# Kernel optimization log

Hardware: AMD Instinct MI355X
Metric: run time of the kernel (lower is better)

## Reference

```python
import jax, jax.numpy as jnp
import numpy as np

B, H, S, D = 4, 16, 2048, 64

def setup_inputs() -> dict:
    key = jax.random.key(0)
    kq, kk, kv = jax.random.split(key, 3)
    q = jax.random.normal(kq, (B, H, S, D), dtype=jnp.float32)
    k = jax.random.normal(kk, (B, H, S, D), dtype=jnp.float32)
    v = jax.random.normal(kv, (B, H, S, D), dtype=jnp.float32)
    return {"q": q, "k": k, "v": v}

def reference(q, k, v):
    # naive unfused attention: scores = QK^T / sqrt(d), softmax, then @ V
    scale = 1.0 / jnp.sqrt(jnp.asarray(q.shape[-1], q.dtype))
    scores = jnp.einsum('bhqd,bhkd->bhqk', q, k) * scale  # [B,H,S,S] materialized
    attn = jax.nn.softmax(scores, axis=-1)
    out = jnp.einsum('bhqk,bhkd->bhqd', attn, v)
    return out
```

## Files before the change

kernel.cpp:

```cpp
#include <hip/hip_runtime.h>


#define S_LEN 2048
#define D_DIM 64
#define N_BH  64
#define QSCALE 0.18033688011112042f

typedef _Float16 half8 __attribute__((ext_vector_type(8)));
typedef _Float16 half4 __attribute__((ext_vector_type(4)));
typedef float floatx16 __attribute__((ext_vector_type(16)));
typedef unsigned int uint4v __attribute__((ext_vector_type(4)));

#define MFMA32(a, b, c) __builtin_amdgcn_mfma_f32_32x32x16_f16((a), (b), (c), 0, 0, 0)

#define GLL16(g, l) __builtin_amdgcn_global_load_lds(                      \
    (const __attribute__((address_space(1))) void*)(g),                    \
    (__attribute__((address_space(3))) void*)(l), 16, 0, 0)

__global__ __launch_bounds__(256) void prep_kernel(
    const float* __restrict__ kg, const float* __restrict__ vg,
    _Float16* __restrict__ kh, _Float16* __restrict__ vt)
{
    __shared__ _Float16 Ls[64 * 132];
    const int tid = threadIdx.x;
    const int bh = blockIdx.y;
    const int sbase = blockIdx.x * 128;
    const size_t gbase = ((size_t)(bh * S_LEN + sbase)) * D_DIM;

#pragma unroll
    for (int i = 0; i < 8; ++i) {
        const int e = i * 1024 + tid * 4;
        const float4 kv = *(const float4*)(kg + gbase + e);
        half4 hk;
        hk[0] = (_Float16)kv.x; hk[1] = (_Float16)kv.y;
        hk[2] = (_Float16)kv.z; hk[3] = (_Float16)kv.w;
        *(half4*)(kh + gbase + e) = hk;
    }
#pragma unroll
    for (int i = 0; i < 8; ++i) {
        const int e = i * 1024 + tid * 4;
        const int s = e >> 6, d0 = e & 63;
        const float4 vv = *(const float4*)(vg + gbase + e);
        const int sp = (s & ~12) | ((s & 4) << 1) | ((s & 8) >> 1);
        Ls[(d0 + 0) * 132 + sp] = (_Float16)vv.x;
        Ls[(d0 + 1) * 132 + sp] = (_Float16)vv.y;
        Ls[(d0 + 2) * 132 + sp] = (_Float16)vv.z;
        Ls[(d0 + 3) * 132 + sp] = (_Float16)vv.w;
    }
    __syncthreads();
    const int w = tid >> 6, L = tid & 63;
    const int dr = L >> 4;
    const int c  = L & 15;
#pragma unroll
    for (int k = 0; k < 4; ++k) {
        const int d = w * 16 + k * 4 + dr;
        const half4 lo = *(const half4*)&Ls[d * 132 + c * 8];
        const half4 hi = *(const half4*)&Ls[d * 132 + c * 8 + 4];
        half8 o;
        o[0] = lo[0]; o[1] = lo[1]; o[2] = lo[2]; o[3] = lo[3];
        o[4] = hi[0]; o[5] = hi[1]; o[6] = hi[2]; o[7] = hi[3];
        *(half8*)(vt + ((size_t)(bh * D_DIM + d)) * S_LEN + sbase + c * 8) = o;
    }
}

__global__ __launch_bounds__(256, 2) void fa_kernel(
    const float* __restrict__ qg, const _Float16* __restrict__ kh,
    const _Float16* __restrict__ vt, float* __restrict__ outg)
{
    __shared__ _Float16 Kl0[64 * 64];
    __shared__ _Float16 Kl1[64 * 64];
    __shared__ _Float16 Vl0[64 * 64];
    __shared__ _Float16 Vl1[64 * 64];

    const int tid = threadIdx.x;
    const int w = tid >> 6;
    const int L = tid & 63;
    const int lq = L & 31;
    const int h = L >> 5;

    const int id = blockIdx.x;
    const int bh   = ((id & 7) << 3) | (id >> 6);
    const int qblk = (id >> 3) & 7;
    const int qrowA = qblk * 256 + w * 32 + lq;

    half8 qbA[4], qbB[4];
    {
        const float* qpA = qg + ((size_t)bh * S_LEN + qrowA) * D_DIM + h * 8;
        const float* qpB = qpA + 128 * D_DIM;
#pragma unroll
        for (int ks = 0; ks < 4; ++ks) {
            const float4 a0 = *(const float4*)(qpA + ks * 16);
            const float4 b0 = *(const float4*)(qpA + ks * 16 + 4);
            const float4 a1 = *(const float4*)(qpB + ks * 16);
            const float4 b1 = *(const float4*)(qpB + ks * 16 + 4);
            qbA[ks][0] = (_Float16)(a0.x * QSCALE);
            qbA[ks][1] = (_Float16)(a0.y * QSCALE);
            qbA[ks][2] = (_Float16)(a0.z * QSCALE);
            qbA[ks][3] = (_Float16)(a0.w * QSCALE);
            qbA[ks][4] = (_Float16)(b0.x * QSCALE);
            qbA[ks][5] = (_Float16)(b0.y * QSCALE);
            qbA[ks][6] = (_Float16)(b0.z * QSCALE);
            qbA[ks][7] = (_Float16)(b0.w * QSCALE);
            qbB[ks][0] = (_Float16)(a1.x * QSCALE);
            qbB[ks][1] = (_Float16)(a1.y * QSCALE);
            qbB[ks][2] = (_Float16)(a1.z * QSCALE);
            qbB[ks][3] = (_Float16)(a1.w * QSCALE);
            qbB[ks][4] = (_Float16)(b1.x * QSCALE);
            qbB[ks][5] = (_Float16)(b1.y * QSCALE);
            qbB[ks][6] = (_Float16)(b1.z * QSCALE);
            qbB[ks][7] = (_Float16)(b1.w * QSCALE);
        }
    }

    floatx16 o0A, o1A, lacA, o0B, o1B, lacB;
#pragma unroll
    for (int r = 0; r < 16; ++r) {
        o0A[r] = 0.f; o1A[r] = 0.f; lacA[r] = 0.f;
        o0B[r] = 0.f; o1B[r] = 0.f; lacB[r] = 0.f;
    }

    half8 ones;
#pragma unroll
    for (int j = 0; j < 8; ++j) ones[j] = (_Float16)1.0f;

    const int rloc = L >> 3, lc = L & 7;
    const int crd = lc ^ rloc;
    const _Float16* kgl = kh + (size_t)bh * S_LEN * D_DIM
                        + (size_t)(w * 16 + rloc) * D_DIM + crd * 8;
    const _Float16* vgl = vt + (size_t)bh * D_DIM * S_LEN
                        + (size_t)(w * 16 + rloc) * S_LEN + crd * 8;
    const int woff = w * 16 * 64;

#define STAGE(KD, VD) do {                                                 \
        GLL16(kgl,                     &KD[woff]);                         \
        GLL16(kgl + (size_t)8 * D_DIM, &KD[woff + 8 * 64]);                \
        GLL16(vgl,                     &VD[woff]);                         \
        GLL16(vgl + (size_t)8 * S_LEN, &VD[woff + 8 * 64]);                \
        kgl += 64 * D_DIM;                                                 \
        vgl += 64;                                                         \
    } while (0)

#define COMPUTE(KB, VB) do {                                               \
                 \
        floatx16 s0A, s1A, s0B, s1B;                                       \
        _Pragma("unroll")                                                  \
        for (int r = 0; r < 16; ++r) {                                     \
            s0A[r] = 0.f; s1A[r] = 0.f; s0B[r] = 0.f; s1B[r] = 0.f;        \
        }                                                                  \
        __builtin_amdgcn_s_setprio(1);                                     \
        _Pragma("unroll")                                                  \
        for (int ks = 0; ks < 4; ++ks) {                                   \
            const int sw = (((2 * ks + h) ^ (lq & 7)) << 3);               \
            const half8 ka0 = *(const half8*)&KB[lq * 64 + sw];            \
            const half8 ka1 = *(const half8*)&KB[(32 + lq) * 64 + sw];     \
            s0A = MFMA32(ka0, qbA[ks], s0A);                               \
            s1A = MFMA32(ka1, qbA[ks], s1A);                               \
            s0B = MFMA32(ka0, qbB[ks], s0B);                               \
            s1B = MFMA32(ka1, qbB[ks], s1B);                               \
        }                                                                  \
        __builtin_amdgcn_s_setprio(0);                                     \
                           \
        unsigned int pkA0[8], pkA1[8], pkB0[8], pkB1[8];                   \
        _Pragma("unroll")                                                  \
        for (int p = 0; p < 8; ++p) {                                      \
            const auto eA0 = __builtin_amdgcn_cvt_pkrtz(                   \
                __builtin_amdgcn_exp2f(s0A[2 * p]),                        \
                __builtin_amdgcn_exp2f(s0A[2 * p + 1]));                   \
            const auto eA1 = __builtin_amdgcn_cvt_pkrtz(                   \
                __builtin_amdgcn_exp2f(s1A[2 * p]),                        \
                __builtin_amdgcn_exp2f(s1A[2 * p + 1]));                   \
            pkA0[p] = __builtin_bit_cast(unsigned int, eA0);               \
            pkA1[p] = __builtin_bit_cast(unsigned int, eA1);               \
        }                                                                  \
        _Pragma("unroll")                                                  \
        for (int p = 0; p < 8; ++p) {                                      \
            const auto eB0 = __builtin_amdgcn_cvt_pkrtz(                   \
                __builtin_amdgcn_exp2f(s0B[2 * p]),                        \
                __builtin_amdgcn_exp2f(s0B[2 * p + 1]));                   \
            const auto eB1 = __builtin_amdgcn_cvt_pkrtz(                   \
                __builtin_amdgcn_exp2f(s1B[2 * p]),                        \
                __builtin_amdgcn_exp2f(s1B[2 * p + 1]));                   \
            pkB0[p] = __builtin_bit_cast(unsigned int, eB0);               \
            pkB1[p] = __builtin_bit_cast(unsigned int, eB1);               \
        }                                                                  \
            \
        __builtin_amdgcn_s_setprio(1);                                     \
        _Pragma("unroll")                                                  \
        for (int mt = 0; mt < 2; ++mt) {                                   \
            const unsigned int* pA = mt ? pkA1 : pkA0;                     \
            const unsigned int* pB = mt ? pkB1 : pkB0;                     \
            const uint4v uA0 = {pA[0], pA[1], pA[2], pA[3]};               \
            const uint4v uA1 = {pA[4], pA[5], pA[6], pA[7]};               \
            const uint4v uB0 = {pB[0], pB[1], pB[2], pB[3]};               \
            const uint4v uB1 = {pB[4], pB[5], pB[6], pB[7]};               \
            const half8 afA0 = __builtin_bit_cast(half8, uA0);             \
            const half8 afA1 = __builtin_bit_cast(half8, uA1);             \
            const half8 afB0 = __builtin_bit_cast(half8, uB0);             \
            const half8 afB1 = __builtin_bit_cast(half8, uB1);             \
            lacA = MFMA32(afA0 + afA1, ones, lacA);                        \
            lacB = MFMA32(afB0 + afB1, ones, lacB);                        \
            _Pragma("unroll")                                              \
            for (int kl = 0; kl < 2; ++kl) {                               \
                const int ksg = mt * 2 + kl;                               \
                const int sw = (((2 * ksg + h) ^ (lq & 7)) << 3);          \
                const half8 vb0 = *(const half8*)&VB[lq * 64 + sw];        \
                const half8 vb1 = *(const half8*)&VB[(32 + lq) * 64 + sw]; \
                const half8 afA = kl ? afA1 : afA0;                        \
                const half8 afB = kl ? afB1 : afB0;                        \
                o0A = MFMA32(afA, vb0, o0A);                               \
                o1A = MFMA32(afA, vb1, o1A);                               \
                o0B = MFMA32(afB, vb0, o0B);                               \
                o1B = MFMA32(afB, vb1, o1B);                               \
            }                                                              \
        }                                                                  \
        __builtin_amdgcn_s_setprio(0);                                     \
    } while (0)

    STAGE(Kl0, Vl0);
    __syncthreads();

    for (int it = 0; it < 15; ++it) {
        STAGE(Kl1, Vl1);
        COMPUTE(Kl0, Vl0);
        __syncthreads();
        STAGE(Kl0, Vl0);
        COMPUTE(Kl1, Vl1);
        __syncthreads();
    }
    STAGE(Kl1, Vl1);
    COMPUTE(Kl0, Vl0);
    __syncthreads();
    COMPUTE(Kl1, Vl1);

#undef STAGE
#undef COMPUTE

    float* obA = outg + ((size_t)bh * S_LEN + qblk * 256 + w * 32) * D_DIM;
    float* obB = obA + (size_t)128 * D_DIM;
#pragma unroll
    for (int reg = 0; reg < 16; ++reg) {
        const int q = (reg & 3) + 8 * (reg >> 2) + 4 * h;
        const float invA = 1.0f / lacA[reg];
        const float invB = 1.0f / lacB[reg];
        obA[(size_t)q * D_DIM + lq]      = o0A[reg] * invA;
        obA[(size_t)q * D_DIM + 32 + lq] = o1A[reg] * invA;
        obB[(size_t)q * D_DIM + lq]      = o0B[reg] * invB;
        obB[(size_t)q * D_DIM + 32 + lq] = o1B[reg] * invB;
    }
}

extern "C" void kernel_launch(void* const* d_in, const int* in_sizes, int n_in,
                              void* d_out, int out_size, void* d_ws, size_t ws_size,
                              hipStream_t stream) {
    const float* q = (const float*)d_in[0];
    const float* k = (const float*)d_in[1];
    const float* v = (const float*)d_in[2];
    float* out = (float*)d_out;
    (void)in_sizes; (void)n_in; (void)out_size; (void)ws_size;

    _Float16* kh = (_Float16*)d_ws;
    _Float16* vt = kh + (size_t)N_BH * S_LEN * D_DIM;

    prep_kernel<<<dim3(S_LEN / 128, N_BH), dim3(256), 0, stream>>>(k, v, kh, vt);
    fa_kernel<<<dim3(512), dim3(256), 0, stream>>>(q, kh, vt, out);
}
```

Before: 200.3 us.

## Split KV sequence across two blocks with atomic-flag combine

Adds a split-KV mode: each (bh, qblk) tile is processed by two blocks, each covering half of the keys. Both write unnormalized partial outputs and row sums to workspace, and the second block to finish, found through an atomic counter, sums the two halves and normalizes. This doubles the grid from 512 to 1024 blocks so more CUs are busy, at the cost of extra global traffic for the partials and a combine step. The mode is enabled only when the workspace is large enough, and the flags are reset in the prep kernel.

```diff
diff --git a/kernel.cpp b/kernel.cpp
--- a/kernel.cpp
+++ b/kernel.cpp
@@ -19,13 +19,16 @@
 
 __global__ __launch_bounds__(256) void prep_kernel(
     const float* __restrict__ kg, const float* __restrict__ vg,
-    _Float16* __restrict__ kh, _Float16* __restrict__ vt)
+    _Float16* __restrict__ kh, _Float16* __restrict__ vt,
+    int* __restrict__ flags, int nhalf)
 {
     __shared__ _Float16 Ls[64 * 132];
     const int tid = threadIdx.x;
     const int bh = blockIdx.y;
     const int sbase = blockIdx.x * 128;
     const size_t gbase = ((size_t)(bh * S_LEN + sbase)) * D_DIM;
+
+    if (nhalf == 2 && blockIdx.x == 0 && tid < 8) flags[(bh << 3) | tid] = 0;
 
 #pragma unroll
     for (int i = 0; i < 8; ++i) {
@@ -65,12 +68,15 @@
 
 __global__ __launch_bounds__(256, 2) void fa_kernel(
     const float* __restrict__ qg, const _Float16* __restrict__ kh,
-    const _Float16* __restrict__ vt, float* __restrict__ outg)
+    const _Float16* __restrict__ vt, float* __restrict__ outg,
+    float* __restrict__ op, float* __restrict__ lacp,
+    int* __restrict__ flags, int nhalf)
 {
     __shared__ _Float16 Kl0[64 * 64];
     __shared__ _Float16 Kl1[64 * 64];
     __shared__ _Float16 Vl0[64 * 64];
     __shared__ _Float16 Vl1[64 * 64];
+    __shared__ int role;
 
     const int tid = threadIdx.x;
     const int w = tid >> 6;
@@ -79,9 +85,11 @@
     const int h = L >> 5;
 
     const int id = blockIdx.x;
-    const int bh   = ((id & 7) << 3) | (id >> 6);
-    const int qblk = (id >> 3) & 7;
+    const int bh   = ((id & 7) << 3) | ((id >> 3) & 7);
+    const int qblk = (id >> 6) & 7;
+    const int kvh  = (id >> 9) & 1;
     const int qrowA = qblk * 256 + w * 32 + lq;
+    const int kbase = kvh * (S_LEN / 2);
 
     half8 qbA[4], qbB[4];
     {
@@ -126,9 +134,9 @@
     const int rloc = L >> 3, lc = L & 7;
     const int crd = lc ^ rloc;
     const _Float16* kgl = kh + (size_t)bh * S_LEN * D_DIM
-                        + (size_t)(w * 16 + rloc) * D_DIM + crd * 8;
+                        + (size_t)(kbase + w * 16 + rloc) * D_DIM + crd * 8;
     const _Float16* vgl = vt + (size_t)bh * D_DIM * S_LEN
-                        + (size_t)(w * 16 + rloc) * S_LEN + crd * 8;
+                        + (size_t)(w * 16 + rloc) * S_LEN + kbase + crd * 8;
     const int woff = w * 16 * 64;
 
 #define STAGE(KD, VD) do {                                                 \
@@ -219,7 +227,8 @@
     STAGE(Kl0, Vl0);
     __syncthreads();
 
-    for (int it = 0; it < 15; ++it) {
+    const int niter = (nhalf == 2) ? 7 : 15;
+    for (int it = 0; it < niter; ++it) {
         STAGE(Kl1, Vl1);
         COMPUTE(Kl0, Vl0);
         __syncthreads();
@@ -235,17 +244,61 @@
 #undef STAGE
 #undef COMPUTE
 
-    float* obA = outg + ((size_t)bh * S_LEN + qblk * 256 + w * 32) * D_DIM;
-    float* obB = obA + (size_t)128 * D_DIM;
-#pragma unroll
-    for (int reg = 0; reg < 16; ++reg) {
-        const int q = (reg & 3) + 8 * (reg >> 2) + 4 * h;
-        const float invA = 1.0f / lacA[reg];
-        const float invB = 1.0f / lacB[reg];
-        obA[(size_t)q * D_DIM + lq]      = o0A[reg] * invA;
-        obA[(size_t)q * D_DIM + 32 + lq] = o1A[reg] * invA;
-        obB[(size_t)q * D_DIM + lq]      = o0B[reg] * invB;
-        obB[(size_t)q * D_DIM + 32 + lq] = o1B[reg] * invB;
+    const size_t qoff = (size_t)bh * S_LEN + qblk * 256 + w * 32;
+
+    if (nhalf == 1) {
+        float* obA = outg + qoff * D_DIM;
+        float* obB = obA + (size_t)128 * D_DIM;
+#pragma unroll
+        for (int reg = 0; reg < 16; ++reg) {
+            const int q = (reg & 3) + 8 * (reg >> 2) + 4 * h;
+            const float invA = 1.0f / lacA[reg];
+            const float invB = 1.0f / lacB[reg];
+            obA[(size_t)q * D_DIM + lq]      = o0A[reg] * invA;
+            obA[(size_t)q * D_DIM + 32 + lq] = o1A[reg] * invA;
+            obB[(size_t)q * D_DIM + lq]      = o0B[reg] * invB;
+            obB[(size_t)q * D_DIM + 32 + lq] = o1B[reg] * invB;
+        }
+        return;
+    }
+
+    {
+        const size_t HOP = (size_t)N_BH * S_LEN * D_DIM;
+        const size_t HLC = (size_t)N_BH * S_LEN;
+        float* pb = op + (size_t)kvh * HOP + qoff * D_DIM;
+        float* pl = lacp + (size_t)kvh * HLC + qoff;
+#pragma unroll
+        for (int reg = 0; reg < 16; ++reg) {
+            const int q = (reg & 3) + 8 * (reg >> 2) + 4 * h;
+            pb[(size_t)q * D_DIM + lq]              = o0A[reg];
+            pb[(size_t)q * D_DIM + 32 + lq]         = o1A[reg];
+            pb[(size_t)(128 + q) * D_DIM + lq]      = o0B[reg];
+            pb[(size_t)(128 + q) * D_DIM + 32 + lq] = o1B[reg];
+            if (lq == 0) { pl[q] = lacA[reg]; pl[128 + q] = lacB[reg]; }
+        }
+        __threadfence();
+        __syncthreads();
+        if (tid == 0) role = atomicAdd(&flags[(bh << 3) | qblk], 1);
+        __syncthreads();
+        if (role == 1) {
+            const float* qb_ = op + (size_t)(kvh ^ 1) * HOP + qoff * D_DIM;
+            const float* ql_ = lacp + (size_t)(kvh ^ 1) * HLC + qoff;
+            float* ob = outg + qoff * D_DIM;
+#pragma unroll
+            for (int reg = 0; reg < 16; ++reg) {
+                const int q = (reg & 3) + 8 * (reg >> 2) + 4 * h;
+                const float invA = 1.0f / (lacA[reg] + ql_[q]);
+                const float invB = 1.0f / (lacB[reg] + ql_[128 + q]);
+                ob[(size_t)q * D_DIM + lq] =
+                    (o0A[reg] + qb_[(size_t)q * D_DIM + lq]) * invA;
+                ob[(size_t)q * D_DIM + 32 + lq] =
+                    (o1A[reg] + qb_[(size_t)q * D_DIM + 32 + lq]) * invA;
+                ob[(size_t)(128 + q) * D_DIM + lq] =
+                    (o0B[reg] + qb_[(size_t)(128 + q) * D_DIM + lq]) * invB;
+                ob[(size_t)(128 + q) * D_DIM + 32 + lq] =
+                    (o1B[reg] + qb_[(size_t)(128 + q) * D_DIM + 32 + lq]) * invB;
+            }
+        }
     }
 }
 
@@ -256,11 +309,23 @@
     const float* k = (const float*)d_in[1];
     const float* v = (const float*)d_in[2];
     float* out = (float*)d_out;
-    (void)in_sizes; (void)n_in; (void)out_size; (void)ws_size;
+    (void)in_sizes; (void)n_in; (void)out_size;
+
+    const size_t KH = (size_t)N_BH * S_LEN * D_DIM * 2;
+    const size_t OP = (size_t)2 * N_BH * S_LEN * D_DIM * 4;
+    const size_t LC = (size_t)2 * N_BH * S_LEN * 4;
+    const size_t need = 2 * KH + OP + LC + 2048;
 
     _Float16* kh = (_Float16*)d_ws;
-    _Float16* vt = kh + (size_t)N_BH * S_LEN * D_DIM;
-
-    prep_kernel<<<dim3(S_LEN / 128, N_BH), dim3(256), 0, stream>>>(k, v, kh, vt);
-    fa_kernel<<<dim3(512), dim3(256), 0, stream>>>(q, kh, vt, out);
+    _Float16* vt = (_Float16*)((char*)d_ws + KH);
+    float* op    = (float*)((char*)d_ws + 2 * KH);
+    float* lacp  = (float*)((char*)d_ws + 2 * KH + OP);
+    int*   flags = (int*)((char*)d_ws + 2 * KH + OP + LC);
+
+    const int nhalf = (ws_size >= need) ? 2 : 1;
+
+    prep_kernel<<<dim3(S_LEN / 128, N_BH), dim3(256), 0, stream>>>(
+        k, v, kh, vt, flags, nhalf);
+    fa_kernel<<<dim3(512 * nhalf), dim3(256), 0, stream>>>(
+        q, kh, vt, out, op, lacp, flags, nhalf);
 }
```

Result: slower. 350.4 us (+74.9%).
